# Kernel tuning notes

Hardware: AMD Instinct MI355X
Metric: run time of the kernel (lower is better)

## Reference

```python
import jax, jax.numpy as jnp
import numpy as np
from jax import lax

B, U, W, E, H, Hh, C = 16, 64, 32, 300, 512, 512, 7
D = 2 * H  # bidirectional LSTM feature size


def setup_inputs() -> dict:
    key = jax.random.key(0)
    ks = jax.random.split(key, 24)
    rn = lambda k, s, sc=0.05: jax.random.normal(k, s, jnp.float32) * sc
    z = lambda n: jnp.zeros((n,), jnp.float32)
    return {
        "x": jax.random.normal(ks[0], (B, U, W, E), jnp.float32),
        # BiLSTM (PyTorch gate order i,f,g,o)
        "lstm_Wih_f": rn(ks[1], (4 * H, E)), "lstm_Whh_f": rn(ks[2], (4 * H, H)),
        "lstm_bih_f": z(4 * H), "lstm_bhh_f": z(4 * H),
        "lstm_Wih_b": rn(ks[3], (4 * H, E)), "lstm_Whh_b": rn(ks[4], (4 * H, H)),
        "lstm_bih_b": z(4 * H), "lstm_bhh_b": z(4 * H),
        # global_state_gru (GRUCell, gate order r,z,n)
        "gg_Wih": rn(ks[5], (3 * D, D)), "gg_Whh": rn(ks[6], (3 * D, D)),
        "gg_bih": z(3 * D), "gg_bhh": z(3 * D),
        # attention weight
        "Wg": rn(ks[7], (D, D)),
        # party_state_gru
        "pg_Wih": rn(ks[8], (3 * D, D)), "pg_Whh": rn(ks[9], (3 * D, D)),
        "pg_bih": z(3 * D), "pg_bhh": z(3 * D),
        # emotion_state_gru
        "eg_Wih": rn(ks[10], (3 * Hh, D)), "eg_Whh": rn(ks[11], (3 * Hh, Hh)),
        "eg_bih": z(3 * Hh), "eg_bhh": z(3 * Hh),
        # classifier
        "cls_W": rn(ks[12], (C, Hh)), "cls_b": z(C),
    }


def _gru_cell(x, h, Wih, Whh, bih, bhh):
    gi = x @ Wih.T + bih
    gh = h @ Whh.T + bhh
    ir, iz, inn = jnp.split(gi, 3, axis=-1)
    hr, hz, hn = jnp.split(gh, 3, axis=-1)
    r = jax.nn.sigmoid(ir + hr)
    zg = jax.nn.sigmoid(iz + hz)
    n = jnp.tanh(inn + r * hn)
    return (1.0 - zg) * n + zg * h


def _lstm(xs, Wih, Whh, bih, bhh, reverse):
    # xs: [W, N, E]; returns hidden states [W, N, H] in scan order
    if reverse:
        xs = xs[::-1]
    N = xs.shape[1]
    def step(carry, xt):
        h, c = carry
        g = xt @ Wih.T + bih + h @ Whh.T + bhh
        i, f, gg, o = jnp.split(g, 4, axis=-1)
        c = jax.nn.sigmoid(f) * c + jax.nn.sigmoid(i) * jnp.tanh(gg)
        h = jax.nn.sigmoid(o) * jnp.tanh(c)
        return (h, c), h
    init = (jnp.zeros((N, H), xs.dtype), jnp.zeros((N, H), xs.dtype))
    _, hs = lax.scan(step, init, xs)
    return hs


def reference(x, lstm_Wih_f, lstm_Whh_f, lstm_bih_f, lstm_bhh_f,
              lstm_Wih_b, lstm_Whh_b, lstm_bih_b, lstm_bhh_b,
              gg_Wih, gg_Whh, gg_bih, gg_bhh, Wg,
              pg_Wih, pg_Whh, pg_bih, pg_bhh,
              eg_Wih, eg_Whh, eg_bih, eg_bhh, cls_W, cls_b):
    # --- extract_features: BiLSTM over words, fwd last step + bwd first step ---
    N = B * U
    xs = jnp.swapaxes(x.reshape(N, W, E), 0, 1)  # [W, N, E]
    hf = _lstm(xs, lstm_Wih_f, lstm_Whh_f, lstm_bih_f, lstm_bhh_f, False)[-1]  # fwd @ t=W-1
    hb = _lstm(xs, lstm_Wih_b, lstm_Whh_b, lstm_bih_b, lstm_bhh_b, True)[-1]   # bwd @ t=0
    feat = jnp.concatenate([hf, hb], axis=-1).reshape(B, U, D)

    # --- detect_emotions: sequential GRU recurrence with growing-history attention ---
    utt = jnp.swapaxes(feat, 0, 1)  # [U, B, D]
    tpos = jnp.arange(U + 1)

    def step(carry, sx):
        hist, p0, p1, e = carry  # hist: [U+1, B, D], hist[0] = zeros
        u, i = sx
        is0 = (i % 2) == 0
        p = jnp.where(is0, p0, p1)
        g_new = _gru_cell(u + p, hist[i], gg_Wih, gg_Whh, gg_bih, gg_bhh)
        hist = hist.at[i + 1].set(g_new)
        # attention over history states 0..i (excludes just-appended g_new)
        q = u @ Wg                                  # [B, D]
        scores = jnp.einsum('bd,tbd->tb', q, hist)  # [U+1, B]
        scores = jnp.where((tpos <= i)[:, None], scores, -1e9)
        w = jax.nn.softmax(scores, axis=0)
        ctx = jnp.einsum('tb,tbd->bd', w, hist)
        p_new = _gru_cell(u + ctx, p, pg_Wih, pg_Whh, pg_bih, pg_bhh)
        p0 = jnp.where(is0, p_new, p0)
        p1 = jnp.where(is0, p1, p_new)
        e = _gru_cell(p_new, e, eg_Wih, eg_Whh, eg_bih, eg_bhh)
        return (hist, p0, p1, e), e

    init = (jnp.zeros((U + 1, B, D), feat.dtype),
            jnp.zeros((B, D), feat.dtype),
            jnp.zeros((B, D), feat.dtype),
            jnp.zeros((B, Hh), feat.dtype))
    _, es = lax.scan(step, init, (utt, jnp.arange(U)))  # es: [U, B, Hh]

    out = jnp.swapaxes(es, 0, 1) @ cls_W.T + cls_b  # [B, U, C]
    return out
```

## Files before the change

### kernel.cpp

```cpp
#include <hip/hip_runtime.h>
#include <hip/hip_bf16.h>


#define DEV static __device__ __forceinline__

typedef __attribute__((ext_vector_type(4))) float f32x4;
typedef __attribute__((ext_vector_type(8))) short bf16x8;
typedef __attribute__((ext_vector_type(8))) unsigned short u16x8;

DEV float sigmoidf_(float x) { return 1.0f / (1.0f + __expf(-x)); }

DEV unsigned short f2bf(float f) {
    union { float f; unsigned u; } v; v.f = f;
    unsigned r = v.u + 0x7FFFu + ((v.u >> 16) & 1u);
    return (unsigned short)(r >> 16);
}

DEV bf16x8 cvt8(f32x4 a, f32x4 b) {
    bf16x8 r;
    r[0] = (short)f2bf(a[0]); r[1] = (short)f2bf(a[1]);
    r[2] = (short)f2bf(a[2]); r[3] = (short)f2bf(a[3]);
    r[4] = (short)f2bf(b[0]); r[5] = (short)f2bf(b[1]);
    r[6] = (short)f2bf(b[2]); r[7] = (short)f2bf(b[3]);
    return r;
}


__global__ __launch_bounds__(256) void k_build_xpad(const float* __restrict__ x,
                                                    unsigned short* __restrict__ xpad) {
    size_t gt = (size_t)blockIdx.x * 256 + threadIdx.x;
    if (gt >= (size_t)20971520) return;
    int kp = (int)(gt % 320);
    int n = (int)((gt / 320) & 1023);
    int t = (int)((gt / (320 * 1024)) & 31);
    int dir = (int)(gt / ((size_t)320 * 1024 * 32));
    int teff = dir ? (31 - t) : t;
    float v = (kp < 300) ? x[((size_t)n * 32 + teff) * 300 + kp] : 0.0f;
    xpad[gt] = f2bf(v);
}

__global__ __launch_bounds__(256) void k_build_wcat(
    const float* __restrict__ wihf, const float* __restrict__ whhf,
    const float* __restrict__ wihb, const float* __restrict__ whhb,
    unsigned short* __restrict__ wcat) {
    int gt = blockIdx.x * 256 + threadIdx.x;
    if (gt >= 2 * 2048 * 832) return;
    int k = gt % 832;
    int j = (gt / 832) & 2047;
    int dir = gt / (832 * 2048);
    const float* wih = dir ? wihb : wihf;
    const float* whh = dir ? whhb : whhf;
    float v = 0.0f;
    if (k < 300) v = wih[j * 300 + k];
    else if (k >= 320) v = whh[j * 512 + (k - 320)];
    wcat[gt] = f2bf(v);
}

__global__ __launch_bounds__(256) void k_cat_w(const float* __restrict__ Wih,
                                               const float* __restrict__ Whh,
                                               unsigned short* __restrict__ out,
                                               int K1, int K2) {
    int j = blockIdx.x;
    int KW = K1 + K2;
    const float* a = Wih + (size_t)j * K1;
    const float* b = Whh + (size_t)j * K2;
    unsigned short* o = out + (size_t)j * KW;
    for (int k = threadIdx.x; k < KW; k += 256)
        o[k] = f2bf(k < K1 ? a[k] : b[k - K1]);
}

__global__ __launch_bounds__(256) void k_transpose_bf(const float* __restrict__ in,
                                                      unsigned short* __restrict__ out) {
    __shared__ float t[64][65];
    int tid = threadIdx.x;
    int r0 = blockIdx.y * 64, c0 = blockIdx.x * 64;
#pragma unroll
    for (int rep = 0; rep < 16; ++rep) {
        int lin = rep * 256 + tid;
        int r = lin >> 6, c = lin & 63;
        t[r][c] = in[(size_t)(r0 + r) * 1024 + c0 + c];
    }
    __syncthreads();
#pragma unroll
    for (int rep = 0; rep < 16; ++rep) {
        int lin = rep * 256 + tid;
        int d = lin >> 6, k = lin & 63;
        out[(size_t)(c0 + d) * 1024 + r0 + k] = f2bf(t[k][d]);
    }
}


__global__ __launch_bounds__(256) void k_lstm_gemm(
    const unsigned short* __restrict__ xpad,
    const unsigned short* __restrict__ hbf,
    const unsigned short* __restrict__ wcat,
    float* __restrict__ gates,
    int t) {
    __shared__ unsigned short As[64][72];
    __shared__ unsigned short Ws[64][72];

    const int tid  = threadIdx.x;
    const int br   = blockIdx.x;
    const int bc   = blockIdx.y;
    const int row0 = br * 64;
    const int dir  = row0 >> 10;
    const int n0   = row0 & 1023;
    const int col0 = bc * 64;

    const int lane = tid & 63;
    const int wv   = tid >> 6;
    const int wm   = (wv >> 1) * 32;
    const int wn   = (wv & 1) * 32;
    const int srow = tid >> 2;
    const int sk0  = (tid & 3) * 16;
    const int arow = lane & 15;
    const int kq   = (lane >> 4) * 8;

    f32x4 acc[2][2];
#pragma unroll
    for (int i = 0; i < 2; ++i)
#pragma unroll
        for (int j = 0; j < 2; ++j) acc[i][j] = (f32x4){0.f, 0.f, 0.f, 0.f};

    const unsigned short* xrow = xpad + (((size_t)dir * 32 + t) * 1024 + n0 + srow) * 320;
    const unsigned short* hrow = hbf + ((size_t)dir * 1024 + n0 + srow) * 512;
    const unsigned short* wrp  = wcat + ((size_t)dir * 2048 + col0 + srow) * 832;

    for (int kt = 0; kt < 13; ++kt) {
        const unsigned short* asrc = (kt < 5) ? (xrow + kt * 64) : (hrow + (kt * 64 - 320));
        const unsigned short* wsrc = wrp + kt * 64;
        *(u16x8*)&As[srow][sk0]     = *(const u16x8*)&asrc[sk0];
        *(u16x8*)&As[srow][sk0 + 8] = *(const u16x8*)&asrc[sk0 + 8];
        *(u16x8*)&Ws[srow][sk0]     = *(const u16x8*)&wsrc[sk0];
        *(u16x8*)&Ws[srow][sk0 + 8] = *(const u16x8*)&wsrc[sk0 + 8];
        __syncthreads();
#pragma unroll
        for (int kk = 0; kk < 64; kk += 32) {
            bf16x8 af[2], bfg[2];
#pragma unroll
            for (int i = 0; i < 2; ++i) {
                af[i]  = *(const bf16x8*)&As[wm + i * 16 + arow][kk + kq];
                bfg[i] = *(const bf16x8*)&Ws[wn + i * 16 + arow][kk + kq];
            }
#pragma unroll
            for (int i = 0; i < 2; ++i)
#pragma unroll
                for (int j = 0; j < 2; ++j)
                    acc[i][j] = __builtin_amdgcn_mfma_f32_16x16x32_bf16(
                        af[i], bfg[j], acc[i][j], 0, 0, 0);
        }
        __syncthreads();
    }

    const int rrow = (lane >> 4) * 4;
    const int ccol = lane & 15;
    float* gout = gates + (size_t)dir * 1024 * 2048;
#pragma unroll
    for (int i = 0; i < 2; ++i)
#pragma unroll
        for (int j = 0; j < 2; ++j) {
            int nrw = n0 + wm + i * 16 + rrow;
            int cl  = col0 + wn + j * 16 + ccol;
#pragma unroll
            for (int r = 0; r < 4; ++r)
                gout[(size_t)(nrw + r) * 2048 + cl] = acc[i][j][r];
        }
}

__global__ __launch_bounds__(256) void k_lstm_point(
    const float* __restrict__ gates, float* __restrict__ c, float* __restrict__ h,
    unsigned short* __restrict__ hbf,
    const float* __restrict__ bihf, const float* __restrict__ bhhf,
    const float* __restrict__ bihb, const float* __restrict__ bhhb) {
    int gt = blockIdx.x * 256 + threadIdx.x;
    int j   = gt & 511;
    int n   = (gt >> 9) & 1023;
    int dir = gt >> 19;
    const float* g   = gates + (size_t)dir * 1024 * 2048 + (size_t)n * 2048;
    const float* bih = dir ? bihb : bihf;
    const float* bhh = dir ? bhhb : bhhf;
    float iv = g[j]        + bih[j]        + bhh[j];
    float fv = g[j + 512]  + bih[j + 512]  + bhh[j + 512];
    float gv = g[j + 1024] + bih[j + 1024] + bhh[j + 1024];
    float ov = g[j + 1536] + bih[j + 1536] + bhh[j + 1536];
    size_t idx = (size_t)dir * 524288 + (size_t)n * 512 + j;
    float cv = sigmoidf_(fv) * c[idx] + sigmoidf_(iv) * tanhf(gv);
    float hv = sigmoidf_(ov) * tanhf(cv);
    c[idx] = cv;
    h[idx] = hv;
    hbf[idx] = f2bf(hv);
}

__global__ __launch_bounds__(256) void k_feat(const float* __restrict__ h,
                                              float* __restrict__ feat,
                                              unsigned short* __restrict__ featbf) {
    int idx = blockIdx.x * 256 + threadIdx.x;
    int n = idx >> 10;
    int d = idx & 1023;
    float v = (d < 512) ? h[(size_t)n * 512 + d]
                        : h[524288 + (size_t)n * 512 + (d - 512)];
    feat[idx] = v;
    featbf[idx] = f2bf(v);
}

__global__ __launch_bounds__(256) void k_gemm_bt(
    const unsigned short* __restrict__ A, int lda,
    const unsigned short* __restrict__ B, int ldb,
    float* __restrict__ C, int ldc, int K) {
    __shared__ unsigned short As[64][72];
    __shared__ unsigned short Bs[64][72];
    const int tid = threadIdx.x;
    const int m0 = blockIdx.x * 64;
    const int n0 = blockIdx.y * 64;
    const int lane = tid & 63;
    const int wvq = tid >> 6;
    const int wm = (wvq >> 1) * 32;
    const int wn = (wvq & 1) * 32;
    const int srow = tid >> 2;
    const int sk0 = (tid & 3) * 16;
    const int arow = lane & 15;
    const int kq = (lane >> 4) * 8;
    f32x4 acc[2][2];
#pragma unroll
    for (int i = 0; i < 2; ++i)
#pragma unroll
        for (int j = 0; j < 2; ++j) acc[i][j] = (f32x4){0.f, 0.f, 0.f, 0.f};
    const unsigned short* ar = A + (size_t)(m0 + srow) * lda;
    const unsigned short* br = B + (size_t)(n0 + srow) * ldb;
    for (int kb = 0; kb < K; kb += 64) {
        int k0 = kb + sk0;
        *(u16x8*)&As[srow][sk0]     = *(const u16x8*)&ar[k0];
        *(u16x8*)&As[srow][sk0 + 8] = *(const u16x8*)&ar[k0 + 8];
        *(u16x8*)&Bs[srow][sk0]     = *(const u16x8*)&br[k0];
        *(u16x8*)&Bs[srow][sk0 + 8] = *(const u16x8*)&br[k0 + 8];
        __syncthreads();
#pragma unroll
        for (int kk = 0; kk < 64; kk += 32) {
            bf16x8 af[2], bfg[2];
#pragma unroll
            for (int i = 0; i < 2; ++i) {
                af[i]  = *(const bf16x8*)&As[wm + i * 16 + arow][kk + kq];
                bfg[i] = *(const bf16x8*)&Bs[wn + i * 16 + arow][kk + kq];
            }
#pragma unroll
            for (int i = 0; i < 2; ++i)
#pragma unroll
                for (int j = 0; j < 2; ++j)
                    acc[i][j] = __builtin_amdgcn_mfma_f32_16x16x32_bf16(
                        af[i], bfg[j], acc[i][j], 0, 0, 0);
        }
        __syncthreads();
    }
    const int rrow = (lane >> 4) * 4;
    const int ccol = lane & 15;
#pragma unroll
    for (int i = 0; i < 2; ++i)
#pragma unroll
        for (int j = 0; j < 2; ++j) {
            int mr = m0 + wm + i * 16 + rrow;
            int nc = n0 + wn + j * 16 + ccol;
#pragma unroll
            for (int r = 0; r < 4; ++r)
                C[(size_t)(mr + r) * ldc + nc] = acc[i][j][r];
        }
}


DEV void gru_block16(
    int c0,
    const float* __restrict__ aBase, long aStride,
    const float* __restrict__ addBase, long addStride,
    const float* __restrict__ hBase, long hStride,
    const unsigned short* __restrict__ W,
    const float* __restrict__ bih, const float* __restrict__ bhh,
    float* __restrict__ outBase, long outStride,
    int D, int K1, int K2,
    float (*sred)[3][16][17]) {
    const int tid = threadIdx.x;
    const int lane = tid & 63;
    const int wv = tid >> 6;
    const int p = lane & 15;
    const int kq = (lane >> 4) * 8;
    const int KW = K1 + K2;
    const int Kc = KW >> 4;
    const int kStart = wv * Kc;
    const bool hasAdd = (addBase != nullptr);

    f32x4 accA[3], accB[3];
#pragma unroll
    for (int g = 0; g < 3; ++g) {
        accA[g] = (f32x4){0.f, 0.f, 0.f, 0.f};
        accB[g] = (f32x4){0.f, 0.f, 0.f, 0.f};
    }
    const unsigned short* w0 = W + (size_t)(c0 + p) * KW;
    const unsigned short* w1 = w0 + (size_t)D * KW;
    const unsigned short* w2 = w1 + (size_t)D * KW;
    const float* aRow = aBase + (size_t)p * aStride;
    const float* addRow = hasAdd ? addBase + (size_t)p * addStride : (const float*)0;
    const float* hRow = hBase + (size_t)p * hStride;

    for (int k = kStart; k < kStart + Kc; k += 32) {
        const int kk = k + kq;
        f32x4 x0, x1;
        const bool inA = (k < K1);
        if (inA) {
            x0 = *(const f32x4*)&aRow[kk];
            x1 = *(const f32x4*)&aRow[kk + 4];
            if (hasAdd) {
                f32x4 y0 = *(const f32x4*)&addRow[kk];
                f32x4 y1 = *(const f32x4*)&addRow[kk + 4];
                x0 = x0 + y0; x1 = x1 + y1;
            }
        } else {
            x0 = *(const f32x4*)&hRow[kk - K1];
            x1 = *(const f32x4*)&hRow[kk - K1 + 4];
        }
        bf16x8 af = cvt8(x0, x1);
        bf16x8 b0 = *(const bf16x8*)&w0[kk];
        bf16x8 b1 = *(const bf16x8*)&w1[kk];
        bf16x8 b2 = *(const bf16x8*)&w2[kk];
        if (inA) {
            accA[0] = __builtin_amdgcn_mfma_f32_16x16x32_bf16(af, b0, accA[0], 0, 0, 0);
            accA[1] = __builtin_amdgcn_mfma_f32_16x16x32_bf16(af, b1, accA[1], 0, 0, 0);
            accA[2] = __builtin_amdgcn_mfma_f32_16x16x32_bf16(af, b2, accA[2], 0, 0, 0);
        } else {
            accB[0] = __builtin_amdgcn_mfma_f32_16x16x32_bf16(af, b0, accB[0], 0, 0, 0);
            accB[1] = __builtin_amdgcn_mfma_f32_16x16x32_bf16(af, b1, accB[1], 0, 0, 0);
            accB[2] = __builtin_amdgcn_mfma_f32_16x16x32_bf16(af, b2, accB[2], 0, 0, 0);
        }
    }

    const int mB = (lane >> 4) * 4;
    const int m = tid >> 4;
    const int d = tid & 15;

#pragma unroll
    for (int g = 0; g < 3; ++g)
#pragma unroll
        for (int r = 0; r < 4; ++r)
            sred[wv][g][mB + r][p] = accA[g][r];
    __syncthreads();
    float ir = 0.f, iz = 0.f, inn = 0.f;
    if (tid < 256) {
#pragma unroll
        for (int w = 0; w < 16; ++w) {
            ir += sred[w][0][m][d]; iz += sred[w][1][m][d]; inn += sred[w][2][m][d];
        }
    }
    __syncthreads();
#pragma unroll
    for (int g = 0; g < 3; ++g)
#pragma unroll
        for (int r = 0; r < 4; ++r)
            sred[wv][g][mB + r][p] = accB[g][r];
    __syncthreads();
    if (tid < 256) {
        float hr = 0.f, hz = 0.f, hn = 0.f;
#pragma unroll
        for (int w = 0; w < 16; ++w) {
            hr += sred[w][0][m][d]; hz += sred[w][1][m][d]; hn += sred[w][2][m][d];
        }
        int gd = c0 + d;
        float rg = sigmoidf_(ir + bih[gd] + hr + bhh[gd]);
        float zg = sigmoidf_(iz + bih[gd + D] + hz + bhh[gd + D]);
        float ng = tanhf(inn + bih[gd + 2 * D] + rg * (hn + bhh[gd + 2 * D]));
        float hp = hBase[(size_t)m * hStride + gd];
        outBase[(size_t)m * outStride + gd] = (1.0f - zg) * ng + zg * hp;
    }
}

DEV void attn_block(int b, int i, const float* __restrict__ q_all,
                    const float* __restrict__ hist, float* __restrict__ ctxout,
                    float* __restrict__ satt) {
    const int tid = threadIdx.x;
    const int lane = tid & 63;
    const int wv = tid >> 6;
    const float* qb = q_all + ((size_t)b * 64 + i) * 1024;
    for (int t = wv; t <= i; t += 16) {
        const float* hrow = hist + ((size_t)t * 16 + b) * 1024;
        float s = 0.f;
        for (int dd = lane; dd < 1024; dd += 64) s += qb[dd] * hrow[dd];
        for (int o = 32; o > 0; o >>= 1) s += __shfl_down(s, o);
        if (lane == 0) satt[t] = s;
    }
    __syncthreads();
    if (wv == 0) {
        float v = (lane <= i) ? satt[lane] : -3.0e38f;
        float mx = v;
        for (int o = 32; o > 0; o >>= 1) mx = fmaxf(mx, __shfl_xor(mx, o));
        float e = (lane <= i) ? __expf(v - mx) : 0.f;
        float sum = e;
        for (int o = 32; o > 0; o >>= 1) sum += __shfl_xor(sum, o);
        if (lane <= i) satt[lane] = e / sum;
    }
    __syncthreads();
    const int dd = tid;
    float s = 0.f;
    for (int t = 0; t <= i; ++t)
        s += satt[t] * hist[((size_t)t * 16 + b) * 1024 + dd];
    ctxout[(size_t)b * 1024 + dd] = s;
}

__global__ __launch_bounds__(1024) void k_dec_A(
    const float* __restrict__ feat, const float* __restrict__ q_all,
    float* __restrict__ hist, const float* __restrict__ psel,
    const unsigned short* __restrict__ ggW,
    const float* __restrict__ gg_bih, const float* __restrict__ gg_bhh,
    float* __restrict__ ctxb,
    const float* __restrict__ pn_prev, const float* __restrict__ e_prev,
    float* __restrict__ es_prev_out,
    const unsigned short* __restrict__ egW,
    const float* __restrict__ eg_bih, const float* __restrict__ eg_bhh,
    int i) {
    __shared__ float sred[16][3][16][17];
    __shared__ float satt[80];
    const int blk = blockIdx.x;
    if (blk < 64) {
        if (i >= 64) return;
        gru_block16(blk * 16, feat + (size_t)i * 1024, 65536L, psel, 1024L,
                    hist + (size_t)i * 16384, 1024L, ggW, gg_bih, gg_bhh,
                    hist + (size_t)(i + 1) * 16384, 1024L, 1024, 1024, 1024, sred);
    } else if (blk < 80) {
        if (i >= 64) return;
        attn_block(blk - 64, i, q_all, hist, ctxb, satt);
    } else {
        if (i < 1) return;
        gru_block16((blk - 80) * 16, pn_prev, 1024L, (const float*)0, 0L,
                    e_prev, 512L, egW, eg_bih, eg_bhh,
                    es_prev_out, 512L, 512, 1024, 512, sred);
    }
}

__global__ __launch_bounds__(1024) void k_dec_B(
    const float* __restrict__ feat, const float* __restrict__ ctxb,
    const float* __restrict__ psel,
    const unsigned short* __restrict__ pgW,
    const float* __restrict__ pg_bih, const float* __restrict__ pg_bhh,
    float* __restrict__ pn, int i) {
    __shared__ float sred[16][3][16][17];
    gru_block16(blockIdx.x * 16, feat + (size_t)i * 1024, 65536L, ctxb, 1024L,
                psel, 1024L, pgW, pg_bih, pg_bhh, pn, 1024L, 1024, 1024, 1024, sred);
}

__global__ __launch_bounds__(256) void k_cls(const float* __restrict__ es,
                                             const float* __restrict__ W,
                                             const float* __restrict__ bias,
                                             float* __restrict__ out) {
    int blk = blockIdx.x;
    int b = blk >> 6;
    int u = blk & 63;
    const float* erow = es + ((size_t)u * 16 + b) * 512;
    int tid = threadIdx.x;
    int lane = tid & 63;
    int wv = tid >> 6;
    for (int c = wv; c < 7; c += 4) {
        float s = 0.f;
        for (int k = lane; k < 512; k += 64) s += erow[k] * W[(size_t)c * 512 + k];
        for (int o = 32; o > 0; o >>= 1) s += __shfl_down(s, o);
        if (lane == 0) out[((size_t)b * 64 + u) * 7 + c] = s + bias[c];
    }
}


extern "C" void kernel_launch(void* const* d_in, const int* in_sizes, int n_in,
                              void* d_out, int out_size, void* d_ws, size_t ws_size,
                              hipStream_t stream) {
    (void)in_sizes; (void)n_in; (void)out_size; (void)ws_size;
    const float* x          = (const float*)d_in[0];
    const float* lstm_Wih_f = (const float*)d_in[1];
    const float* lstm_Whh_f = (const float*)d_in[2];
    const float* lstm_bih_f = (const float*)d_in[3];
    const float* lstm_bhh_f = (const float*)d_in[4];
    const float* lstm_Wih_b = (const float*)d_in[5];
    const float* lstm_Whh_b = (const float*)d_in[6];
    const float* lstm_bih_b = (const float*)d_in[7];
    const float* lstm_bhh_b = (const float*)d_in[8];
    const float* gg_Wih = (const float*)d_in[9];
    const float* gg_Whh = (const float*)d_in[10];
    const float* gg_bih = (const float*)d_in[11];
    const float* gg_bhh = (const float*)d_in[12];
    const float* Wg     = (const float*)d_in[13];
    const float* pg_Wih = (const float*)d_in[14];
    const float* pg_Whh = (const float*)d_in[15];
    const float* pg_bih = (const float*)d_in[16];
    const float* pg_bhh = (const float*)d_in[17];
    const float* eg_Wih = (const float*)d_in[18];
    const float* eg_Whh = (const float*)d_in[19];
    const float* eg_bih = (const float*)d_in[20];
    const float* eg_bhh = (const float*)d_in[21];
    const float* cls_W  = (const float*)d_in[22];
    const float* cls_b  = (const float*)d_in[23];

    char* wsp = (char*)d_ws;
    size_t off = 0;
    auto alloc = [&](size_t bytes) -> void* {
        void* p = wsp + off;
        off += (bytes + 255) & ~(size_t)255;
        return p;
    };
    unsigned short* xpad = (unsigned short*)alloc((size_t)20971520 * 2);
    unsigned short* wcat = (unsigned short*)alloc((size_t)2 * 2048 * 832 * 2);
    unsigned short* hbf  = (unsigned short*)alloc((size_t)2 * 1024 * 512 * 2);
    float* hbuf  = (float*)alloc((size_t)2 * 1024 * 512 * 4);
    float* cbuf  = (float*)alloc((size_t)2 * 1024 * 512 * 4);
    float* gates = (float*)alloc((size_t)2 * 1024 * 2048 * 4);
    float* feat  = (float*)alloc((size_t)1024 * 1024 * 4);
    unsigned short* featbf = (unsigned short*)alloc((size_t)1024 * 1024 * 2);
    float* hist  = (float*)alloc((size_t)65 * 16 * 1024 * 4);
    float* q_all = (float*)alloc((size_t)1024 * 1024 * 4);
    float* ctxb  = (float*)alloc((size_t)16 * 1024 * 4);
    float* pnew  = (float*)alloc((size_t)64 * 16 * 1024 * 4);
    float* esb   = (float*)alloc((size_t)64 * 16 * 512 * 4);
    float* zeroD = (float*)alloc((size_t)16 * 1024 * 4);
    float* zeroH = (float*)alloc((size_t)16 * 512 * 4);
    unsigned short* WgTb = (unsigned short*)alloc((size_t)1024 * 1024 * 2);
    unsigned short* ggWb = (unsigned short*)gates;
    unsigned short* pgWb = (unsigned short*)xpad;
    unsigned short* egWb = (unsigned short*)((char*)xpad + 12582912);

    hipMemsetAsync(hbf, 0, (size_t)2 * 1024 * 512 * 2, stream);
    hipMemsetAsync(cbuf, 0, (size_t)2 * 1024 * 512 * 4, stream);
    hipMemsetAsync(hist, 0, (size_t)65 * 16 * 1024 * 4, stream);
    hipMemsetAsync(zeroD, 0, (size_t)16 * 1024 * 4, stream);
    hipMemsetAsync(zeroH, 0, (size_t)16 * 512 * 4, stream);

    k_build_xpad<<<81920, 256, 0, stream>>>(x, xpad);
    k_build_wcat<<<13312, 256, 0, stream>>>(lstm_Wih_f, lstm_Whh_f, lstm_Wih_b, lstm_Whh_b, wcat);

    for (int t = 0; t < 32; ++t) {
        k_lstm_gemm<<<dim3(32, 32), 256, 0, stream>>>(xpad, hbf, wcat, gates, t);
        k_lstm_point<<<4096, 256, 0, stream>>>(gates, cbuf, hbuf, hbf,
                                               lstm_bih_f, lstm_bhh_f, lstm_bih_b, lstm_bhh_b);
    }
    k_feat<<<4096, 256, 0, stream>>>(hbuf, feat, featbf);

    k_cat_w<<<3072, 256, 0, stream>>>(gg_Wih, gg_Whh, ggWb, 1024, 1024);
    k_cat_w<<<3072, 256, 0, stream>>>(pg_Wih, pg_Whh, pgWb, 1024, 1024);
    k_cat_w<<<1536, 256, 0, stream>>>(eg_Wih, eg_Whh, egWb, 1024, 512);
    k_transpose_bf<<<dim3(16, 16), 256, 0, stream>>>(Wg, WgTb);
    k_gemm_bt<<<dim3(16, 16), 256, 0, stream>>>(featbf, 1024, WgTb, 1024, q_all, 1024, 1024);

    float* p0 = zeroD;
    float* p1 = zeroD;
    for (int i = 0; i <= 64; ++i) {
        float* psel = (i & 1) ? p1 : p0;
        const float* pn_prev = (i >= 1) ? pnew + (size_t)(i - 1) * 16384 : (const float*)0;
        const float* e_prev  = (i >= 2) ? esb + (size_t)(i - 2) * 8192 : zeroH;
        float* es_prev_out   = (i >= 1) ? esb + (size_t)(i - 1) * 8192 : (float*)0;
        k_dec_A<<<112, 1024, 0, stream>>>(feat, q_all, hist, psel,
                                          ggWb, gg_bih, gg_bhh, ctxb,
                                          pn_prev, e_prev, es_prev_out,
                                          egWb, eg_bih, eg_bhh, i);
        if (i < 64) {
            float* pn = pnew + (size_t)i * 16384;
            k_dec_B<<<64, 1024, 0, stream>>>(feat, ctxb, psel, pgWb, pg_bih, pg_bhh, pn, i);
            if (i & 1) p1 = pn; else p0 = pn;
        }
    }
    k_cls<<<1024, 256, 0, stream>>>(esb, cls_W, cls_b, (float*)d_out);
}
```

Baseline: 3.120 ms.

## Fuse LSTM gate GEMM with pointwise cell update and double-buffer hidden state

```diff
diff --git a/kernel.cpp b/kernel.cpp
--- a/kernel.cpp
+++ b/kernel.cpp
@@ -28,15 +28,21 @@
 
 __global__ __launch_bounds__(256) void k_build_xpad(const float* __restrict__ x,
                                                     unsigned short* __restrict__ xpad) {
-    size_t gt = (size_t)blockIdx.x * 256 + threadIdx.x;
-    if (gt >= (size_t)20971520) return;
-    int kp = (int)(gt % 320);
-    int n = (int)((gt / 320) & 1023);
-    int t = (int)((gt / (320 * 1024)) & 31);
-    int dir = (int)(gt / ((size_t)320 * 1024 * 32));
+    int g = blockIdx.x * 256 + threadIdx.x;
+    if (g >= 2621440) return;
+    int kg = (g % 40) * 8;
+    int n = (g / 40) & 1023;
+    int t = (g / (40 * 1024)) & 31;
+    int dir = g / (40 * 1024 * 32);
     int teff = dir ? (31 - t) : t;
-    float v = (kp < 300) ? x[((size_t)n * 32 + teff) * 300 + kp] : 0.0f;
-    xpad[gt] = f2bf(v);
+    const float* xr = x + ((size_t)n * 32 + teff) * 300;
+    u16x8 o;
+#pragma unroll
+    for (int e = 0; e < 8; ++e) {
+        int kp = kg + e;
+        o[e] = (kp < 300) ? f2bf(xr[kp]) : (unsigned short)0;
+    }
+    *(u16x8*)&xpad[(size_t)g * 8] = o;
 }
 
 __global__ __launch_bounds__(256) void k_build_wcat(
@@ -90,14 +96,18 @@
 }
 
 
-__global__ __launch_bounds__(256) void k_lstm_gemm(
+__global__ __launch_bounds__(256) void k_lstm_step(
     const unsigned short* __restrict__ xpad,
-    const unsigned short* __restrict__ hbf,
+    const unsigned short* __restrict__ hbfin,
     const unsigned short* __restrict__ wcat,
-    float* __restrict__ gates,
+    float* __restrict__ cbuf,
+    float* __restrict__ hbuf,
+    unsigned short* __restrict__ hbfout,
+    const float* __restrict__ bihf, const float* __restrict__ bhhf,
+    const float* __restrict__ bihb, const float* __restrict__ bhhb,
     int t) {
     __shared__ unsigned short As[64][72];
-    __shared__ unsigned short Ws[64][72];
+    __shared__ unsigned short Ws[4][64][72];
 
     const int tid  = threadIdx.x;
     const int br   = blockIdx.x;
@@ -105,7 +115,7 @@
     const int row0 = br * 64;
     const int dir  = row0 >> 10;
     const int n0   = row0 & 1023;
-    const int col0 = bc * 64;
+    const int j0   = bc * 64;
 
     const int lane = tid & 63;
     const int wv   = tid >> 6;
@@ -116,79 +126,75 @@
     const int arow = lane & 15;
     const int kq   = (lane >> 4) * 8;
 
-    f32x4 acc[2][2];
-#pragma unroll
-    for (int i = 0; i < 2; ++i)
-#pragma unroll
-        for (int j = 0; j < 2; ++j) acc[i][j] = (f32x4){0.f, 0.f, 0.f, 0.f};
+    f32x4 acc[4][2][2];
+#pragma unroll
+    for (int g = 0; g < 4; ++g)
+#pragma unroll
+        for (int i = 0; i < 2; ++i)
+#pragma unroll
+            for (int j = 0; j < 2; ++j) acc[g][i][j] = (f32x4){0.f, 0.f, 0.f, 0.f};
 
     const unsigned short* xrow = xpad + (((size_t)dir * 32 + t) * 1024 + n0 + srow) * 320;
-    const unsigned short* hrow = hbf + ((size_t)dir * 1024 + n0 + srow) * 512;
-    const unsigned short* wrp  = wcat + ((size_t)dir * 2048 + col0 + srow) * 832;
+    const unsigned short* hrow = hbfin + ((size_t)dir * 1024 + n0 + srow) * 512;
+    const unsigned short* wr0 = wcat + ((size_t)dir * 2048 + j0 + srow) * 832;
 
     for (int kt = 0; kt < 13; ++kt) {
         const unsigned short* asrc = (kt < 5) ? (xrow + kt * 64) : (hrow + (kt * 64 - 320));
-        const unsigned short* wsrc = wrp + kt * 64;
         *(u16x8*)&As[srow][sk0]     = *(const u16x8*)&asrc[sk0];
         *(u16x8*)&As[srow][sk0 + 8] = *(const u16x8*)&asrc[sk0 + 8];
-        *(u16x8*)&Ws[srow][sk0]     = *(const u16x8*)&wsrc[sk0];
-        *(u16x8*)&Ws[srow][sk0 + 8] = *(const u16x8*)&wsrc[sk0 + 8];
+#pragma unroll
+        for (int g = 0; g < 4; ++g) {
+            const unsigned short* wsrc = wr0 + (size_t)g * 512 * 832 + kt * 64;
+            *(u16x8*)&Ws[g][srow][sk0]     = *(const u16x8*)&wsrc[sk0];
+            *(u16x8*)&Ws[g][srow][sk0 + 8] = *(const u16x8*)&wsrc[sk0 + 8];
+        }
         __syncthreads();
 #pragma unroll
         for (int kk = 0; kk < 64; kk += 32) {
-            bf16x8 af[2], bfg[2];
-#pragma unroll
-            for (int i = 0; i < 2; ++i) {
-                af[i]  = *(const bf16x8*)&As[wm + i * 16 + arow][kk + kq];
-                bfg[i] = *(const bf16x8*)&Ws[wn + i * 16 + arow][kk + kq];
+            bf16x8 af[2];
+            af[0] = *(const bf16x8*)&As[wm + arow][kk + kq];
+            af[1] = *(const bf16x8*)&As[wm + 16 + arow][kk + kq];
+#pragma unroll
+            for (int g = 0; g < 4; ++g) {
+                bf16x8 b0 = *(const bf16x8*)&Ws[g][wn + arow][kk + kq];
+                bf16x8 b1 = *(const bf16x8*)&Ws[g][wn + 16 + arow][kk + kq];
+                acc[g][0][0] = __builtin_amdgcn_mfma_f32_16x16x32_bf16(af[0], b0, acc[g][0][0], 0, 0, 0);
+                acc[g][0][1] = __builtin_amdgcn_mfma_f32_16x16x32_bf16(af[0], b1, acc[g][0][1], 0, 0, 0);
+                acc[g][1][0] = __builtin_amdgcn_mfma_f32_16x16x32_bf16(af[1], b0, acc[g][1][0], 0, 0, 0);
+                acc[g][1][1] = __builtin_amdgcn_mfma_f32_16x16x32_bf16(af[1], b1, acc[g][1][1], 0, 0, 0);
             }
-#pragma unroll
-            for (int i = 0; i < 2; ++i)
-#pragma unroll
-                for (int j = 0; j < 2; ++j)
-                    acc[i][j] = __builtin_amdgcn_mfma_f32_16x16x32_bf16(
-                        af[i], bfg[j], acc[i][j], 0, 0, 0);
         }
         __syncthreads();
     }
 
+    const float* bih = dir ? bihb : bihf;
+    const float* bhh = dir ? bhhb : bhhf;
     const int rrow = (lane >> 4) * 4;
     const int ccol = lane & 15;
-    float* gout = gates + (size_t)dir * 1024 * 2048;
 #pragma unroll
     for (int i = 0; i < 2; ++i)
 #pragma unroll
         for (int j = 0; j < 2; ++j) {
-            int nrw = n0 + wm + i * 16 + rrow;
-            int cl  = col0 + wn + j * 16 + ccol;
-#pragma unroll
-            for (int r = 0; r < 4; ++r)
-                gout[(size_t)(nrw + r) * 2048 + cl] = acc[i][j][r];
-        }
-}
-
-__global__ __launch_bounds__(256) void k_lstm_point(
-    const float* __restrict__ gates, float* __restrict__ c, float* __restrict__ h,
-    unsigned short* __restrict__ hbf,
-    const float* __restrict__ bihf, const float* __restrict__ bhhf,
-    const float* __restrict__ bihb, const float* __restrict__ bhhb) {
-    int gt = blockIdx.x * 256 + threadIdx.x;
-    int j   = gt & 511;
-    int n   = (gt >> 9) & 1023;
-    int dir = gt >> 19;
-    const float* g   = gates + (size_t)dir * 1024 * 2048 + (size_t)n * 2048;
-    const float* bih = dir ? bihb : bihf;
-    const float* bhh = dir ? bhhb : bhhf;
-    float iv = g[j]        + bih[j]        + bhh[j];
-    float fv = g[j + 512]  + bih[j + 512]  + bhh[j + 512];
-    float gv = g[j + 1024] + bih[j + 1024] + bhh[j + 1024];
-    float ov = g[j + 1536] + bih[j + 1536] + bhh[j + 1536];
-    size_t idx = (size_t)dir * 524288 + (size_t)n * 512 + j;
-    float cv = sigmoidf_(fv) * c[idx] + sigmoidf_(iv) * tanhf(gv);
-    float hv = sigmoidf_(ov) * tanhf(cv);
-    c[idx] = cv;
-    h[idx] = hv;
-    hbf[idx] = f2bf(hv);
+            const int nr = n0 + wm + i * 16 + rrow;
+            const int gd = j0 + wn + j * 16 + ccol;
+            const float bi = bih[gd]        + bhh[gd];
+            const float bf = bih[gd + 512]  + bhh[gd + 512];
+            const float bg = bih[gd + 1024] + bhh[gd + 1024];
+            const float bo = bih[gd + 1536] + bhh[gd + 1536];
+#pragma unroll
+            for (int r = 0; r < 4; ++r) {
+                const float iv = acc[0][i][j][r] + bi;
+                const float fv = acc[1][i][j][r] + bf;
+                const float gv = acc[2][i][j][r] + bg;
+                const float ov = acc[3][i][j][r] + bo;
+                const size_t idx = (size_t)dir * 524288 + (size_t)(nr + r) * 512 + gd;
+                const float cv = sigmoidf_(fv) * cbuf[idx] + sigmoidf_(iv) * tanhf(gv);
+                const float hv = sigmoidf_(ov) * tanhf(cv);
+                cbuf[idx] = cv;
+                hbuf[idx] = hv;
+                hbfout[idx] = f2bf(hv);
+            }
+        }
 }
 
 __global__ __launch_bounds__(256) void k_feat(const float* __restrict__ h,
@@ -500,10 +506,9 @@
     };
     unsigned short* xpad = (unsigned short*)alloc((size_t)20971520 * 2);
     unsigned short* wcat = (unsigned short*)alloc((size_t)2 * 2048 * 832 * 2);
-    unsigned short* hbf  = (unsigned short*)alloc((size_t)2 * 1024 * 512 * 2);
+    unsigned short* hbf2 = (unsigned short*)alloc((size_t)2 * 2 * 1024 * 512 * 2);
     float* hbuf  = (float*)alloc((size_t)2 * 1024 * 512 * 4);
     float* cbuf  = (float*)alloc((size_t)2 * 1024 * 512 * 4);
-    float* gates = (float*)alloc((size_t)2 * 1024 * 2048 * 4);
     float* feat  = (float*)alloc((size_t)1024 * 1024 * 4);
     unsigned short* featbf = (unsigned short*)alloc((size_t)1024 * 1024 * 2);
     float* hist  = (float*)alloc((size_t)65 * 16 * 1024 * 4);
@@ -514,23 +519,24 @@
     float* zeroD = (float*)alloc((size_t)16 * 1024 * 4);
     float* zeroH = (float*)alloc((size_t)16 * 512 * 4);
     unsigned short* WgTb = (unsigned short*)alloc((size_t)1024 * 1024 * 2);
-    unsigned short* ggWb = (unsigned short*)gates;
-    unsigned short* pgWb = (unsigned short*)xpad;
-    unsigned short* egWb = (unsigned short*)((char*)xpad + 12582912);
-
-    hipMemsetAsync(hbf, 0, (size_t)2 * 1024 * 512 * 2, stream);
+    unsigned short* ggWb = (unsigned short*)xpad;
+    unsigned short* pgWb = (unsigned short*)((char*)xpad + 12582912);
+    unsigned short* egWb = (unsigned short*)((char*)xpad + 25165824);
+
+    hipMemsetAsync(hbf2, 0, (size_t)2 * 1024 * 512 * 2, stream);
     hipMemsetAsync(cbuf, 0, (size_t)2 * 1024 * 512 * 4, stream);
     hipMemsetAsync(hist, 0, (size_t)65 * 16 * 1024 * 4, stream);
     hipMemsetAsync(zeroD, 0, (size_t)16 * 1024 * 4, stream);
     hipMemsetAsync(zeroH, 0, (size_t)16 * 512 * 4, stream);
 
-    k_build_xpad<<<81920, 256, 0, stream>>>(x, xpad);
+    k_build_xpad<<<10240, 256, 0, stream>>>(x, xpad);
     k_build_wcat<<<13312, 256, 0, stream>>>(lstm_Wih_f, lstm_Whh_f, lstm_Wih_b, lstm_Whh_b, wcat);
 
+    const size_t HP = (size_t)2 * 1024 * 512;
     for (int t = 0; t < 32; ++t) {
-        k_lstm_gemm<<<dim3(32, 32), 256, 0, stream>>>(xpad, hbf, wcat, gates, t);
-        k_lstm_point<<<4096, 256, 0, stream>>>(gates, cbuf, hbuf, hbf,
-                                               lstm_bih_f, lstm_bhh_f, lstm_bih_b, lstm_bhh_b);
+        k_lstm_step<<<dim3(32, 8), 256, 0, stream>>>(
+            xpad, hbf2 + (t & 1) * HP, wcat, cbuf, hbuf, hbf2 + ((t + 1) & 1) * HP,
+            lstm_bih_f, lstm_bhh_f, lstm_bih_b, lstm_bhh_b, t);
     }
     k_feat<<<4096, 256, 0, stream>>>(hbuf, feat, featbf);
 
```

New measurement: 3.120 ms. About the same (+0.0%).
